# Kernel tuning notes

Measured on AMD Instinct MI355X. Metric: run time of the kernel, lower is better.

The kernel has to match this reference:

```python
import jax, jax.numpy as jnp
import numpy as np


def setup_inputs() -> dict:
    key = jax.random.key(0)
    k1, k2 = jax.random.split(key)
    N, M, D = 16384, 16384, 3
    return {
        "point_cloud1": jax.random.normal(k1, (N, D), dtype=jnp.float32),
        "point_cloud2": jax.random.normal(k2, (M, D), dtype=jnp.float32),
    }


def reference(point_cloud1, point_cloud2):
    # diff: [N, M, D]; dist_matrix: [N, M] of squared euclidean distances
    diff = point_cloud1[:, None, :] - point_cloud2[None, :, :]
    dist_matrix = jnp.sum(diff ** 2, axis=-1)
    min_dist1 = jnp.min(dist_matrix, axis=1)  # for each point in cloud1, nearest in cloud2
    min_dist2 = jnp.min(dist_matrix, axis=0)  # for each point in cloud2, nearest in cloud1
    return jnp.mean(min_dist1) + jnp.mean(min_dist2)
```

## Files before the change

### kernel.cpp

```cpp
#include <hip/hip_runtime.h>
#include <cfloat>

#define BLOCK 256
#define AU 8
#define TS 256
#define KSPLIT 64
#define RBLOCK 256

typedef float f2 __attribute__((ext_vector_type(2)));

__global__ __launch_bounds__(BLOCK, 4) void chamfer_min_kernel(
    const float* __restrict__ pc1, int N,
    const float* __restrict__ pc2, int M,
    float* __restrict__ P1, float* __restrict__ P2)
{
    __shared__ float sxy[TS * 2];
    __shared__ float szh[TS * 2];
    const int tid = threadIdx.x;

    const float* A; const float* B; float* P; int An, Bn;
    if (blockIdx.z == 0) { A = pc1; An = N; B = pc2; Bn = M; P = P1; }
    else                 { A = pc2; An = M; B = pc1; Bn = N; P = P2; }

    const int abase = blockIdx.x * (BLOCK * AU) + tid;
    const int mlen = (Bn + KSPLIT - 1) / KSPLIT;
    const int m0 = blockIdx.y * mlen;
    const int m1 = min(m0 + mlen, Bn);

    f2 nax2[AU], nay2[AU], naz2[AU];
    #pragma unroll
    for (int u = 0; u < AU; ++u) {
        const int ai = abase + u * BLOCK;
        float x = 0.f, y = 0.f, z = 0.f;
        if (ai < An) {
            x = A[(size_t)ai * 3 + 0];
            y = A[(size_t)ai * 3 + 1];
            z = A[(size_t)ai * 3 + 2];
        }
        nax2[u] = (f2){-x, -x};
        nay2[u] = (f2){-y, -y};
        naz2[u] = (f2){-z, -z};
    }

    float mm[AU];
    #pragma unroll
    for (int u = 0; u < AU; ++u) mm[u] = FLT_MAX;

    for (int t0 = m0; t0 < m1; t0 += TS) {
        const int tcount = min(TS, m1 - t0);
        const int padded = (tcount + 1) & ~1;

        for (int j = tid; j < padded; j += BLOCK) {
            const int srcj = min(j, tcount - 1);
            const size_t s = (size_t)(t0 + srcj) * 3;
            float bx = B[s + 0], by = B[s + 1], bz = B[s + 2];
            float h = 0.5f * fmaf(bx, bx, fmaf(by, by, bz * bz));
            const int p = j >> 1, hf = j & 1;
            sxy[p * 4 + 0 + hf] = bx;
            sxy[p * 4 + 2 + hf] = by;
            szh[p * 4 + 0 + hf] = bz;
            szh[p * 4 + 2 + hf] = h;
        }
        __syncthreads();

        const int npair = padded >> 1;
        const float4* __restrict__ qxyp = (const float4*)sxy;
        const float4* __restrict__ qzhp = (const float4*)szh;
        #pragma unroll 4
        for (int p = 0; p < npair; ++p) {
            float4 qxy = qxyp[p];
            float4 qzh = qzhp[p];
            f2 x2; x2.x = qxy.x; x2.y = qxy.y;
            f2 y2; y2.x = qxy.z; y2.y = qxy.w;
            f2 z2; z2.x = qzh.x; z2.y = qzh.y;
            f2 h2; h2.x = qzh.z; h2.y = qzh.w;
            #pragma unroll
            for (int u = 0; u < AU; ++u) {
                f2 acc;
                asm("v_pk_fma_f32 %0, %1, %2, %3"
                    : "=v"(acc) : "v"(naz2[u]), "v"(z2), "v"(h2));
                asm("v_pk_fma_f32 %0, %1, %2, %0"
                    : "+v"(acc) : "v"(nay2[u]), "v"(y2));
                asm("v_pk_fma_f32 %0, %1, %2, %0"
                    : "+v"(acc) : "v"(nax2[u]), "v"(x2));
                mm[u] = fminf(fminf(mm[u], acc.x), acc.y);
            }
        }
        __syncthreads();
    }

    #pragma unroll
    for (int u = 0; u < AU; ++u) {
        const int ai = abase + u * BLOCK;
        if (ai < An) {
            const float x = nax2[u].x, y = nay2[u].x, z = naz2[u].x;
            const float a2 = fmaf(x, x, fmaf(y, y, z * z));
            float d = fmaf(2.0f, mm[u], a2);
            P[(size_t)blockIdx.y * An + ai] = fmaxf(d, 0.0f);
        }
    }
}

__global__ __launch_bounds__(RBLOCK) void chamfer_reduce1_kernel(
    const float* __restrict__ P1, int N,
    const float* __restrict__ P2, int M,
    double* __restrict__ bsum)
{
    const int tid = threadIdx.x;
    const int g = blockIdx.x * RBLOCK + tid;
    double s = 0.0;
    const int T = N + M;
    if (g < T) {
        const float* base; int stride, i; double scale;
        if (g < N) { base = P1; stride = N; i = g;     scale = 1.0 / (double)N; }
        else       { base = P2; stride = M; i = g - N; scale = 1.0 / (double)M; }
        float v = FLT_MAX;
        #pragma unroll 16
        for (int k = 0; k < KSPLIT; ++k)
            v = fminf(v, base[(size_t)k * stride + i]);
        s = (double)v * scale;
    }
    for (int off = 32; off > 0; off >>= 1)
        s += __shfl_down(s, off, 64);
    __shared__ double wsum[RBLOCK / 64];
    if ((tid & 63) == 0) wsum[tid >> 6] = s;
    __syncthreads();
    if (tid == 0) {
        double tot = 0.0;
        #pragma unroll
        for (int w = 0; w < RBLOCK / 64; ++w) tot += wsum[w];
        bsum[blockIdx.x] = tot;
    }
}

__global__ __launch_bounds__(RBLOCK) void chamfer_reduce2_kernel(
    const double* __restrict__ bsum, int nb, float* __restrict__ out)
{
    const int tid = threadIdx.x;
    double s = 0.0;
    for (int i = tid; i < nb; i += RBLOCK) s += bsum[i];
    for (int off = 32; off > 0; off >>= 1)
        s += __shfl_down(s, off, 64);
    __shared__ double wsum[RBLOCK / 64];
    if ((tid & 63) == 0) wsum[tid >> 6] = s;
    __syncthreads();
    if (tid == 0) {
        double tot = 0.0;
        #pragma unroll
        for (int w = 0; w < RBLOCK / 64; ++w) tot += wsum[w];
        out[0] = (float)tot;
    }
}

extern "C" void kernel_launch(void* const* d_in, const int* in_sizes, int n_in,
                              void* d_out, int out_size, void* d_ws, size_t ws_size,
                              hipStream_t stream) {
    const float* pc1 = (const float*)d_in[0];
    const float* pc2 = (const float*)d_in[1];
    const int N = in_sizes[0] / 3;
    const int M = in_sizes[1] / 3;

    float* P1 = (float*)d_ws;
    float* P2 = P1 + (size_t)KSPLIT * N;
    double* bsum = (double*)(P2 + (size_t)KSPLIT * M);
    float* out = (float*)d_out;

    const int maxNM = (N > M) ? N : M;
    const int gx = (maxNM + BLOCK * AU - 1) / (BLOCK * AU);
    dim3 grid(gx, KSPLIT, 2);
    chamfer_min_kernel<<<grid, BLOCK, 0, stream>>>(pc1, N, pc2, M, P1, P2);

    const int gr = (N + M + RBLOCK - 1) / RBLOCK;
    chamfer_reduce1_kernel<<<gr, RBLOCK, 0, stream>>>(P1, N, P2, M, bsum);
    chamfer_reduce2_kernel<<<1, RBLOCK, 0, stream>>>(bsum, gr, out);
}
```

Before: 54.97 us.

## Stream B points via scalar loads from a pre-packed buffer instead of LDS

Adds a prep kernel that packs each pair of points into an 8-float record of x, y, z and half squared norm. The main kernel then reads those records with s_load_dwordx8 into scalar registers, prefetching one record ahead, instead of staging tiles through shared memory with __syncthreads. This removes LDS traffic and block barriers, since every lane uses the same B values. In exchange it adds an extra kernel launch and a serial s_waitcnt on every iteration, and any scalar-load latency that is not hidden stalls the FMA stream.

Result: slower. 65.18 us (+18.6%).

```diff
diff --git a/kernel.cpp b/kernel.cpp
--- a/kernel.cpp
+++ b/kernel.cpp
@@ -3,29 +3,58 @@
 
 #define BLOCK 256
 #define AU 8
-#define TS 256
 #define KSPLIT 64
 #define RBLOCK 256
 
 typedef float f2 __attribute__((ext_vector_type(2)));
+typedef float f8 __attribute__((ext_vector_type(8)));
+
+__device__ __forceinline__ f8 sload8(const float* p) {
+    f8 r;
+    asm volatile("s_load_dwordx8 %0, %1, 0x0" : "=s"(r) : "s"(p));
+    return r;
+}
+#define LGKM0() do { asm volatile("s_waitcnt lgkmcnt(0)" ::: "memory"); \
+                     __builtin_amdgcn_sched_barrier(0); } while (0)
+
+__global__ __launch_bounds__(256) void prep_kernel(
+    const float* __restrict__ pc1, int N,
+    const float* __restrict__ pc2, int M,
+    float* __restrict__ Bp1, float* __restrict__ Bp2)
+{
+    const int i = blockIdx.x * blockDim.x + threadIdx.x;
+    const int C1 = (N + 1) >> 1, C2 = (M + 1) >> 1;
+    const float* src; float* dst; int n, c;
+    if (i < C1)            { src = pc1; dst = Bp1; n = N; c = i; }
+    else if (i < C1 + C2)  { src = pc2; dst = Bp2; n = M; c = i - C1; }
+    else return;
+    const int j0 = 2 * c, j1 = min(2 * c + 1, n - 1);
+    const float x0 = src[3 * j0], y0 = src[3 * j0 + 1], z0 = src[3 * j0 + 2];
+    const float x1 = src[3 * j1], y1 = src[3 * j1 + 1], z1 = src[3 * j1 + 2];
+    const float h0 = 0.5f * fmaf(x0, x0, fmaf(y0, y0, z0 * z0));
+    const float h1 = 0.5f * fmaf(x1, x1, fmaf(y1, y1, z1 * z1));
+    float4* d4 = (float4*)(dst + (size_t)c * 8);
+    d4[0] = make_float4(x0, x1, y0, y1);
+    d4[1] = make_float4(z0, z1, h0, h1);
+}
 
 __global__ __launch_bounds__(BLOCK, 4) void chamfer_min_kernel(
     const float* __restrict__ pc1, int N,
     const float* __restrict__ pc2, int M,
+    const float* __restrict__ Bp1, const float* __restrict__ Bp2,
     float* __restrict__ P1, float* __restrict__ P2)
 {
-    __shared__ float sxy[TS * 2];
-    __shared__ float szh[TS * 2];
     const int tid = threadIdx.x;
 
-    const float* A; const float* B; float* P; int An, Bn;
-    if (blockIdx.z == 0) { A = pc1; An = N; B = pc2; Bn = M; P = P1; }
-    else                 { A = pc2; An = M; B = pc1; Bn = N; P = P2; }
+    const float* A; const float* Bp; float* P; int An, Bn;
+    if (blockIdx.z == 0) { A = pc1; An = N; Bp = Bp2; Bn = M; P = P1; }
+    else                 { A = pc2; An = M; Bp = Bp1; Bn = N; P = P2; }
 
     const int abase = blockIdx.x * (BLOCK * AU) + tid;
-    const int mlen = (Bn + KSPLIT - 1) / KSPLIT;
+    const int mlen = (((Bn + KSPLIT - 1) / KSPLIT) + 1) & ~1;
     const int m0 = blockIdx.y * mlen;
     const int m1 = min(m0 + mlen, Bn);
+    if (m0 >= Bn) return;
 
     f2 nax2[AU], nay2[AU], naz2[AU];
     #pragma unroll
@@ -46,47 +75,29 @@
     #pragma unroll
     for (int u = 0; u < AU; ++u) mm[u] = FLT_MAX;
 
-    for (int t0 = m0; t0 < m1; t0 += TS) {
-        const int tcount = min(TS, m1 - t0);
-        const int padded = (tcount + 1) & ~1;
+    const int c0 = m0 >> 1;
+    const int c1 = (m1 + 1) >> 1;
 
-        for (int j = tid; j < padded; j += BLOCK) {
-            const int srcj = min(j, tcount - 1);
-            const size_t s = (size_t)(t0 + srcj) * 3;
-            float bx = B[s + 0], by = B[s + 1], bz = B[s + 2];
-            float h = 0.5f * fmaf(bx, bx, fmaf(by, by, bz * bz));
-            const int p = j >> 1, hf = j & 1;
-            sxy[p * 4 + 0 + hf] = bx;
-            sxy[p * 4 + 2 + hf] = by;
-            szh[p * 4 + 0 + hf] = bz;
-            szh[p * 4 + 2 + hf] = h;
+    f8 cur = sload8(Bp + (size_t)c0 * 8);
+    LGKM0();
+    for (int c = c0; c < c1; ++c) {
+        const int cn = min(c + 1, c1 - 1);
+        f8 nxt = sload8(Bp + (size_t)cn * 8);
+
+        const f2 xx = (f2){cur[0], cur[1]};
+        const f2 yy = (f2){cur[2], cur[3]};
+        const f2 zz = (f2){cur[4], cur[5]};
+        const f2 hv = (f2){cur[6], cur[7]};
+        #pragma unroll
+        for (int u = 0; u < AU; ++u) {
+            f2 acc = __builtin_elementwise_fma(naz2[u], zz, hv);
+            acc = __builtin_elementwise_fma(nay2[u], yy, acc);
+            acc = __builtin_elementwise_fma(nax2[u], xx, acc);
+            mm[u] = fminf(fminf(mm[u], acc.x), acc.y);
         }
-        __syncthreads();
 
-        const int npair = padded >> 1;
-        const float4* __restrict__ qxyp = (const float4*)sxy;
-        const float4* __restrict__ qzhp = (const float4*)szh;
-        #pragma unroll 4
-        for (int p = 0; p < npair; ++p) {
-            float4 qxy = qxyp[p];
-            float4 qzh = qzhp[p];
-            f2 x2; x2.x = qxy.x; x2.y = qxy.y;
-            f2 y2; y2.x = qxy.z; y2.y = qxy.w;
-            f2 z2; z2.x = qzh.x; z2.y = qzh.y;
-            f2 h2; h2.x = qzh.z; h2.y = qzh.w;
-            #pragma unroll
-            for (int u = 0; u < AU; ++u) {
-                f2 acc;
-                asm("v_pk_fma_f32 %0, %1, %2, %3"
-                    : "=v"(acc) : "v"(naz2[u]), "v"(z2), "v"(h2));
-                asm("v_pk_fma_f32 %0, %1, %2, %0"
-                    : "+v"(acc) : "v"(nay2[u]), "v"(y2));
-                asm("v_pk_fma_f32 %0, %1, %2, %0"
-                    : "+v"(acc) : "v"(nax2[u]), "v"(x2));
-                mm[u] = fminf(fminf(mm[u], acc.x), acc.y);
-            }
-        }
-        __syncthreads();
+        LGKM0();
+        cur = nxt;
     }
 
     #pragma unroll
@@ -159,16 +170,22 @@
     const float* pc2 = (const float*)d_in[1];
     const int N = in_sizes[0] / 3;
     const int M = in_sizes[1] / 3;
+    const int C1 = (N + 1) >> 1, C2 = (M + 1) >> 1;
 
-    float* P1 = (float*)d_ws;
-    float* P2 = P1 + (size_t)KSPLIT * N;
+    float* Bp1 = (float*)d_ws;
+    float* Bp2 = Bp1 + (size_t)C1 * 8;
+    float* P1  = Bp2 + (size_t)C2 * 8;
+    float* P2  = P1 + (size_t)KSPLIT * N;
     double* bsum = (double*)(P2 + (size_t)KSPLIT * M);
     float* out = (float*)d_out;
+
+    const int cTot = C1 + C2;
+    prep_kernel<<<(cTot + 255) / 256, 256, 0, stream>>>(pc1, N, pc2, M, Bp1, Bp2);
 
     const int maxNM = (N > M) ? N : M;
     const int gx = (maxNM + BLOCK * AU - 1) / (BLOCK * AU);
     dim3 grid(gx, KSPLIT, 2);
-    chamfer_min_kernel<<<grid, BLOCK, 0, stream>>>(pc1, N, pc2, M, P1, P2);
+    chamfer_min_kernel<<<grid, BLOCK, 0, stream>>>(pc1, N, pc2, M, Bp1, Bp2, P1, P2);
 
     const int gr = (N + M + RBLOCK - 1) / RBLOCK;
     chamfer_reduce1_kernel<<<gr, RBLOCK, 0, stream>>>(P1, N, P2, M, bsum);
```
